# Optimization experiments

Hardware: AMD Instinct MI355X
Metric: run time of the kernel (lower is better)

Reference implementation:

```python
import jax, jax.numpy as jnp
import numpy as np

N_HEADS, D_MODEL, D_HEAD = 16, 1024, 64
INIT_STD = 0.02


def setup_inputs() -> dict:
    key = jax.random.key(0)
    ks = jax.random.split(key, 5)
    x = jax.random.normal(ks[0], (4, 2048, D_MODEL), dtype=jnp.float32)
    W_Q = jax.random.normal(ks[1], (N_HEADS, D_MODEL, D_HEAD), dtype=jnp.float32) * INIT_STD
    W_K = jax.random.normal(ks[2], (N_HEADS, D_MODEL, D_HEAD), dtype=jnp.float32) * INIT_STD
    W_V = jax.random.normal(ks[3], (N_HEADS, D_MODEL, D_HEAD), dtype=jnp.float32) * INIT_STD
    W_O = jax.random.normal(ks[4], (N_HEADS, D_HEAD, D_MODEL), dtype=jnp.float32) * INIT_STD
    b_Q = jnp.zeros((N_HEADS, D_HEAD), dtype=jnp.float32)
    b_K = jnp.zeros((N_HEADS, D_HEAD), dtype=jnp.float32)
    b_V = jnp.zeros((N_HEADS, D_HEAD), dtype=jnp.float32)
    b_O = jnp.zeros((D_MODEL,), dtype=jnp.float32)
    return {"normalized_resid_pre": x, "W_Q": W_Q, "W_K": W_K, "W_V": W_V,
            "W_O": W_O, "b_Q": b_Q, "b_K": b_K, "b_V": b_V, "b_O": b_O}


def reference(normalized_resid_pre, W_Q, W_K, W_V, W_O, b_Q, b_K, b_V, b_O):
    x = normalized_resid_pre  # [b, s, d_model]
    q = jnp.einsum('bsm,hmd->bshd', x, W_Q) + b_Q  # [b, s, h, d_head]
    k = jnp.einsum('bsm,hmd->bshd', x, W_K) + b_K
    v = jnp.einsum('bsm,hmd->bshd', x, W_V) + b_V
    scores = jnp.einsum('bqhd,bkhd->bhqk', q, k) / jnp.sqrt(jnp.float32(D_HEAD))
    S = x.shape[1]
    causal = jnp.tril(jnp.ones((S, S), dtype=bool))  # keep key_pos <= query_pos
    scores = jnp.where(causal, scores, jnp.finfo(scores.dtype).min)
    pattern = jax.nn.softmax(scores, axis=-1)  # [b, h, q, k]
    z = jnp.einsum('bhqk,bkhd->bqhd', pattern, v)
    attn_out = jnp.einsum('bqhd,hdm->bqm', z, W_O) + b_O
    return attn_out
```

## Files before the change

kernel.cpp:

```cpp
#include <hip/hip_runtime.h>
#include <hip/hip_bf16.h>
#include <math.h>

typedef __bf16 bf16_t;
typedef bf16_t bf16x8 __attribute__((ext_vector_type(8)));
typedef float f32x4 __attribute__((ext_vector_type(4)));

#define BB 4
#define SS 2048
#define HH 16
#define DMODEL 1024
#define DHEAD 64

__device__ inline unsigned short f2bf(float f) {
    union { __hip_bfloat16 h; unsigned short u; } cvt;
    cvt.h = __float2bfloat16(f);
    return cvt.u;
}

__device__ __forceinline__ void gll16(const unsigned short* g, unsigned short* l) {
    __builtin_amdgcn_global_load_lds(
        (const __attribute__((address_space(1))) unsigned int*)(g),
        (__attribute__((address_space(3))) unsigned int*)(l), 16, 0, 0);
}


__global__ void pack_x(const float* __restrict__ x, unsigned short* __restrict__ xb) {
    int i = blockIdx.x * 256 + threadIdx.x;
    const float4 v = ((const float4*)x)[i];
    unsigned short o[4] = { f2bf(v.x), f2bf(v.y), f2bf(v.z), f2bf(v.w) };
    *(uint2*)(xb + 4 * (size_t)i) = *(uint2*)o;
}

__global__ void pack_wqkv(const float* __restrict__ wq, const float* __restrict__ wk,
                          const float* __restrict__ wv, unsigned short* __restrict__ out) {
    int idx = blockIdx.x * 256 + threadIdx.x;
    int k  = idx & 1023;
    int n  = idx >> 10;
    int mat = n >> 10;
    int n1 = n & 1023;
    int h = n1 >> 6, d = n1 & 63;
    const float* w = (mat == 0) ? wq : (mat == 1) ? wk : wv;
    out[idx] = f2bf(w[(h << 16) + (k << 6) + d]);
}

__global__ void pack_wo(const float* __restrict__ wo, unsigned short* __restrict__ out) {
    int idx = blockIdx.x * 256 + threadIdx.x;
    int k = idx & 1023, n = idx >> 10;
    out[idx] = f2bf(wo[(k << 10) + n]);
}


__global__ __launch_bounds__(256) void gemm_qkv(
    const unsigned short* __restrict__ xb,
    const unsigned short* __restrict__ wT,
    const float* __restrict__ bq, const float* __restrict__ bk, const float* __restrict__ bv,
    unsigned short* __restrict__ qws, unsigned short* __restrict__ kws,
    unsigned short* __restrict__ vtw)
{
    __shared__ __align__(16) unsigned short lA[128 * 32];
    __shared__ __align__(16) unsigned short lB[128 * 32];
    const int t = threadIdx.x;
    const int lane = t & 63;
    const int w = t >> 6;
    const int quad = lane >> 4;
    const int l15 = lane & 15;
    const int n0 = blockIdx.x * 128;
    const int m0 = blockIdx.y * 128;
    const int wm = (w >> 1) * 64;
    const int wn = (w & 1) * 64;
    const int mat = n0 >> 10;

    f32x4 acc[4][4] = {};

    const int srow = w * 16 + (lane >> 2);
    const int scol = (lane & 3) * 8;
    const unsigned short* Ag0 = xb + (size_t)(m0 + srow) * 1024 + scol;
    const unsigned short* Ag1 = Ag0 + (size_t)64 * 1024;
    const unsigned short* Bg0 = wT + (size_t)(n0 + srow) * 1024 + scol;
    const unsigned short* Bg1 = Bg0 + (size_t)64 * 1024;
    unsigned short* lA0 = lA + (w * 16) * 32;
    unsigned short* lA1 = lA + (64 + w * 16) * 32;
    unsigned short* lB0 = lB + (w * 16) * 32;
    unsigned short* lB1 = lB + (64 + w * 16) * 32;

    if (mat != 2) {
        for (int kt = 0; kt < 1024; kt += 32) {
            __syncthreads();
            gll16(Ag0 + kt, lA0);
            gll16(Ag1 + kt, lA1);
            gll16(Bg0 + kt, lB0);
            gll16(Bg1 + kt, lB1);
            __syncthreads();
            bf16x8 af[4], bfr[4];
#pragma unroll
            for (int i = 0; i < 4; i++) {
                af[i]  = *(const bf16x8*)(lA + (wm + i * 16 + l15) * 32 + quad * 8);
                bfr[i] = *(const bf16x8*)(lB + (wn + i * 16 + l15) * 32 + quad * 8);
            }
#pragma unroll
            for (int i = 0; i < 4; i++)
#pragma unroll
                for (int j = 0; j < 4; j++)
                    acc[i][j] = __builtin_amdgcn_mfma_f32_16x16x32_bf16(bfr[j], af[i], acc[i][j], 0, 0, 0);
        }
        const int b = m0 >> 11;
        const float* bias_p = (mat == 0) ? bq : bk;
        unsigned short* dst = (mat == 0) ? qws : kws;
        const float qscale = (mat == 0) ? 0.125f : 1.0f;
#pragma unroll
        for (int j = 0; j < 4; j++) {
            const int noff = wn + j * 16 + quad * 4;
            const int h = noff >> 6;
            const int hglob = ((n0 & 1023) >> 6) + h;
            const int dbase = noff & 63;
            const float4 bv4 = *(const float4*)(bias_p + hglob * 64 + dbase);
            const float bias_r[4] = { bv4.x, bv4.y, bv4.z, bv4.w };
#pragma unroll
            for (int i = 0; i < 4; i++) {
                const int s = (m0 & 2047) + wm + i * 16 + l15;
                unsigned short pk[4];
#pragma unroll
                for (int r = 0; r < 4; r++) pk[r] = f2bf((acc[i][j][r] + bias_r[r]) * qscale);
                *(uint2*)(dst + (size_t)((b * 16 + hglob) * 2048 + s) * 64 + dbase) = *(uint2*)pk;
            }
        }
    } else {
        for (int kt = 0; kt < 1024; kt += 32) {
            __syncthreads();
            gll16(Ag0 + kt, lA0);
            gll16(Ag1 + kt, lA1);
            gll16(Bg0 + kt, lB0);
            gll16(Bg1 + kt, lB1);
            __syncthreads();
            bf16x8 af[4], bfr[4];
#pragma unroll
            for (int i = 0; i < 4; i++) {
                af[i]  = *(const bf16x8*)(lA + (wm + i * 16 + l15) * 32 + quad * 8);
                bfr[i] = *(const bf16x8*)(lB + (wn + i * 16 + l15) * 32 + quad * 8);
            }
#pragma unroll
            for (int i = 0; i < 4; i++)
#pragma unroll
                for (int j = 0; j < 4; j++)
                    acc[i][j] = __builtin_amdgcn_mfma_f32_16x16x32_bf16(af[i], bfr[j], acc[i][j], 0, 0, 0);
        }
        const int b = m0 >> 11;
#pragma unroll
        for (int j = 0; j < 4; j++) {
            const int n1 = (n0 & 1023) + wn + j * 16 + l15;
            const int h = n1 >> 6, d = n1 & 63;
            const float bias = bv[h * 64 + d];
#pragma unroll
            for (int i = 0; i < 4; i++) {
                const int s0 = (m0 & 2047) + wm + i * 16 + quad * 4;
                unsigned short pk[4];
#pragma unroll
                for (int r = 0; r < 4; r++) pk[r] = f2bf(acc[i][j][r] + bias);
                *(uint2*)(vtw + ((size_t)(b * 16 + h) * 64 + d) * 2048 + s0) = *(uint2*)pk;
            }
        }
    }
}


__global__ __launch_bounds__(256) void attn5(
    const unsigned short* __restrict__ qws,
    const unsigned short* __restrict__ kws,
    const unsigned short* __restrict__ vtw,
    unsigned short* __restrict__ zb)
{
    __shared__ __align__(16) unsigned short Ks[64 * 72];
    __shared__ __align__(16) unsigned short Vs[64 * 72];
    __shared__ __align__(16) unsigned short Ps[4 * 16 * 72];

    const int t = threadIdx.x;
    const int lane = t & 63;
    const int w = t >> 6;
    const int quad = lane >> 4;
    const int l15 = lane & 15;

    const int qt = 15 - (blockIdx.x >> 6);
    const int bh = blockIdx.x & 63;
    const int q0 = qt * 128;
    const int qbase = q0 + w * 32;
    const size_t base = (size_t)bh * SS * DHEAD;
    const unsigned short* Q = qws + base;
    const unsigned short* K = kws + base;
    const unsigned short* Vt = vtw + base;

    bf16x8 qf[2][2];
#pragma unroll
    for (int qt_ = 0; qt_ < 2; qt_++) {
        const unsigned short* qp = Q + (size_t)(qbase + qt_ * 16 + l15) * 64 + quad * 8;
        qf[qt_][0] = *(const bf16x8*)(qp);
        qf[qt_][1] = *(const bf16x8*)(qp + 32);
    }

    f32x4 o[2][4] = {};
    float lsum[2] = {0.f, 0.f};
    unsigned short* Pw = Ps + w * 16 * 72;

    const int sr = t >> 2;
    const int sc = (t & 3) * 8;
    const int nch = qt * 2 + 2;

    for (int c = 0; c < nch; c++) {
        const int kb = c * 64;
        __syncthreads();
        {
            const unsigned short* kp = K + (size_t)(kb + sr) * 64 + sc;
            *(uint4*)(Ks + sr * 72 + sc)      = *(const uint4*)(kp);
            *(uint4*)(Ks + sr * 72 + sc + 32) = *(const uint4*)(kp + 32);
            const unsigned short* vp = Vt + (size_t)sr * 2048 + kb + sc;
            *(uint4*)(Vs + sr * 72 + sc)      = *(const uint4*)(vp);
            *(uint4*)(Vs + sr * 72 + sc + 32) = *(const uint4*)(vp + 32);
        }
        __syncthreads();

        if (kb > qbase + 31) continue;

        f32x4 st[2][4];
#pragma unroll
        for (int sub = 0; sub < 4; sub++) {
            const bf16x8 kf0 = *(const bf16x8*)(Ks + (sub * 16 + l15) * 72 + quad * 8);
            const bf16x8 kf1 = *(const bf16x8*)(Ks + (sub * 16 + l15) * 72 + 32 + quad * 8);
#pragma unroll
            for (int qt_ = 0; qt_ < 2; qt_++) {
                f32x4 sv = {};
                sv = __builtin_amdgcn_mfma_f32_16x16x32_bf16(kf0, qf[qt_][0], sv, 0, 0, 0);
                sv = __builtin_amdgcn_mfma_f32_16x16x32_bf16(kf1, qf[qt_][1], sv, 0, 0, 0);
                st[qt_][sub] = sv;
            }
        }

        uint2 pd[2][4];
        const bool edge = (kb + 63 > qbase);
#pragma unroll
        for (int qt_ = 0; qt_ < 2; qt_++) {
            const int qg = qbase + qt_ * 16 + l15;
            float psum = 0.f;
#pragma unroll
            for (int sub = 0; sub < 4; sub++) {
                float p[4];
#pragma unroll
                for (int r = 0; r < 4; r++) {
                    const int key = kb + sub * 16 + quad * 4 + r;
                    float v = __expf(st[qt_][sub][r]);
                    p[r] = (edge && key > qg) ? 0.f : v;
                    psum += p[r];
                }
                pd[qt_][sub].x = (unsigned)f2bf(p[0]) | ((unsigned)f2bf(p[1]) << 16);
                pd[qt_][sub].y = (unsigned)f2bf(p[2]) | ((unsigned)f2bf(p[3]) << 16);
            }
            lsum[qt_] += psum;
        }

        bf16x8 vf[2][4];
#pragma unroll
        for (int c0 = 0; c0 < 2; c0++)
#pragma unroll
            for (int dt = 0; dt < 4; dt++)
                vf[c0][dt] = *(const bf16x8*)(Vs + (dt * 16 + l15) * 72 + c0 * 32 + quad * 8);

#pragma unroll
        for (int qt_ = 0; qt_ < 2; qt_++) {
#pragma unroll
            for (int sub = 0; sub < 4; sub++)
                *(uint2*)(Pw + l15 * 72 + sub * 16 + quad * 4) = pd[qt_][sub];
            asm volatile("s_waitcnt lgkmcnt(0)" ::: "memory");
#pragma unroll
            for (int c0 = 0; c0 < 2; c0++) {
                const bf16x8 pf = *(const bf16x8*)(Pw + l15 * 72 + c0 * 32 + quad * 8);
#pragma unroll
                for (int dt = 0; dt < 4; dt++)
                    o[qt_][dt] = __builtin_amdgcn_mfma_f32_16x16x32_bf16(vf[c0][dt], pf, o[qt_][dt], 0, 0, 0);
            }
            if (qt_ == 0) asm volatile("s_waitcnt lgkmcnt(0)" ::: "memory");
        }
    }

    const int b = bh >> 4, h = bh & 15;
#pragma unroll
    for (int qt_ = 0; qt_ < 2; qt_++) {
        float v = lsum[qt_];
        v += __shfl_xor(v, 16);
        v += __shfl_xor(v, 32);
        const float inv = 1.0f / v;
        const int q = qbase + qt_ * 16 + l15;
        unsigned short* zrow = zb + (size_t)(b * 2048 + q) * 1024 + h * 64 + quad * 4;
#pragma unroll
        for (int dt = 0; dt < 4; dt++) {
            unsigned short pk[4];
#pragma unroll
            for (int r = 0; r < 4; r++) pk[r] = f2bf(o[qt_][dt][r] * inv);
            *(uint2*)(zrow + dt * 16) = *(uint2*)pk;
        }
    }
}


__global__ __launch_bounds__(256) void gemm_out(
    const unsigned short* __restrict__ zb,
    const unsigned short* __restrict__ wT,
    const float* __restrict__ bo,
    float* __restrict__ out)
{
    __shared__ __align__(16) unsigned short lA[128 * 32];
    __shared__ __align__(16) unsigned short lB[128 * 32];
    const int t = threadIdx.x;
    const int lane = t & 63;
    const int w = t >> 6;
    const int quad = lane >> 4;
    const int l15 = lane & 15;
    const int n0 = blockIdx.x * 128;
    const int m0 = blockIdx.y * 128;
    const int wm = (w >> 1) * 64;
    const int wn = (w & 1) * 64;

    f32x4 acc[4][4] = {};

    const int srow = w * 16 + (lane >> 2);
    const int scol = (lane & 3) * 8;
    const unsigned short* Ag0 = zb + (size_t)(m0 + srow) * 1024 + scol;
    const unsigned short* Ag1 = Ag0 + (size_t)64 * 1024;
    const unsigned short* Bg0 = wT + (size_t)(n0 + srow) * 1024 + scol;
    const unsigned short* Bg1 = Bg0 + (size_t)64 * 1024;
    unsigned short* lA0 = lA + (w * 16) * 32;
    unsigned short* lA1 = lA + (64 + w * 16) * 32;
    unsigned short* lB0 = lB + (w * 16) * 32;
    unsigned short* lB1 = lB + (64 + w * 16) * 32;

    for (int kt = 0; kt < 1024; kt += 32) {
        __syncthreads();
        gll16(Ag0 + kt, lA0);
        gll16(Ag1 + kt, lA1);
        gll16(Bg0 + kt, lB0);
        gll16(Bg1 + kt, lB1);
        __syncthreads();
        bf16x8 af[4], bfr[4];
#pragma unroll
        for (int i = 0; i < 4; i++) {
            af[i]  = *(const bf16x8*)(lA + (wm + i * 16 + l15) * 32 + quad * 8);
            bfr[i] = *(const bf16x8*)(lB + (wn + i * 16 + l15) * 32 + quad * 8);
        }
#pragma unroll
        for (int i = 0; i < 4; i++)
#pragma unroll
            for (int j = 0; j < 4; j++)
                acc[i][j] = __builtin_amdgcn_mfma_f32_16x16x32_bf16(bfr[j], af[i], acc[i][j], 0, 0, 0);
    }

#pragma unroll
    for (int j = 0; j < 4; j++) {
        const int nbase = n0 + wn + j * 16 + quad * 4;
        const float4 bv4 = *(const float4*)(bo + nbase);
#pragma unroll
        for (int i = 0; i < 4; i++) {
            const int s = m0 + wm + i * 16 + l15;
            float4 v;
            v.x = acc[i][j][0] + bv4.x;
            v.y = acc[i][j][1] + bv4.y;
            v.z = acc[i][j][2] + bv4.z;
            v.w = acc[i][j][3] + bv4.w;
            *(float4*)(out + (size_t)s * 1024 + nbase) = v;
        }
    }
}


extern "C" void kernel_launch(void* const* d_in, const int* in_sizes, int n_in,
                              void* d_out, int out_size, void* d_ws, size_t ws_size,
                              hipStream_t stream) {
    const float* x  = (const float*)d_in[0];
    const float* WQ = (const float*)d_in[1];
    const float* WK = (const float*)d_in[2];
    const float* WV = (const float*)d_in[3];
    const float* WO = (const float*)d_in[4];
    const float* bQ = (const float*)d_in[5];
    const float* bK = (const float*)d_in[6];
    const float* bV = (const float*)d_in[7];
    const float* bO = (const float*)d_in[8];
    float* out = (float*)d_out;

    char* ws = (char*)d_ws;
    unsigned short* xb   = (unsigned short*)ws;
    unsigned short* wqkv = (unsigned short*)(ws + (16u << 20));
    unsigned short* woT  = (unsigned short*)(ws + (22u << 20));
    unsigned short* qws  = (unsigned short*)(ws + (24u << 20));
    unsigned short* kws  = (unsigned short*)(ws + (40u << 20));
    unsigned short* vtw  = (unsigned short*)(ws + (56u << 20));
    unsigned short* zbuf = xb;

    pack_x<<<8192, 256, 0, stream>>>(x, xb);
    pack_wqkv<<<(3072 * 1024) / 256, 256, 0, stream>>>(WQ, WK, WV, wqkv);
    pack_wo<<<(1024 * 1024) / 256, 256, 0, stream>>>(WO, woT);
    gemm_qkv<<<dim3(24, 64), 256, 0, stream>>>(xb, wqkv, bQ, bK, bV, qws, kws, vtw);
    attn5<<<1024, 256, 0, stream>>>(qws, kws, vtw, zbuf);
    gemm_out<<<dim3(8, 64), 256, 0, stream>>>(zbuf, woT, bO, out);
}
```

Baseline: 293.0 us.

## Split attention keys across waves, tile weight packing, swizzle GEMM block order

The attention kernel now uses 64-query blocks where each wave handles an interleaved subset of 32-key chunks. Each wave has its own LDS region and needs no block-wide barriers in the main loop, and partial outputs and row sums are reduced through shared memory at the end. Softmax switches to exp2 with the log2e factor folded into the Q scale, and probabilities are packed to bf16 with a byte-permute instead of rounding. Weight packing becomes one LDS-tiled transpose kernel with coalesced reads and writes in place of two strided kernels. Both GEMMs use a 1D grid with grouped block ordering for L2 reuse. In exchange, the change adds an LDS reduction epilogue and uses truncating bf16 conversion for the probabilities.

```diff
diff --git a/kernel.cpp b/kernel.cpp
--- a/kernel.cpp
+++ b/kernel.cpp
@@ -11,11 +11,18 @@
 #define HH 16
 #define DMODEL 1024
 #define DHEAD 64
+#define QSCALE 0.18033688011112042f
 
 __device__ inline unsigned short f2bf(float f) {
     union { __hip_bfloat16 h; unsigned short u; } cvt;
     cvt.h = __float2bfloat16(f);
     return cvt.u;
+}
+
+__device__ __forceinline__ unsigned pack_bf2(float lo, float hi) {
+    unsigned a = __builtin_bit_cast(unsigned, lo);
+    unsigned b = __builtin_bit_cast(unsigned, hi);
+    return __builtin_amdgcn_perm(b, a, 0x07060302);
 }
 
 __device__ __forceinline__ void gll16(const unsigned short* g, unsigned short* l) {
@@ -32,22 +39,56 @@
     *(uint2*)(xb + 4 * (size_t)i) = *(uint2*)o;
 }
 
-__global__ void pack_wqkv(const float* __restrict__ wq, const float* __restrict__ wk,
-                          const float* __restrict__ wv, unsigned short* __restrict__ out) {
-    int idx = blockIdx.x * 256 + threadIdx.x;
-    int k  = idx & 1023;
-    int n  = idx >> 10;
-    int mat = n >> 10;
-    int n1 = n & 1023;
-    int h = n1 >> 6, d = n1 & 63;
-    const float* w = (mat == 0) ? wq : (mat == 1) ? wk : wv;
-    out[idx] = f2bf(w[(h << 16) + (k << 6) + d]);
-}
-
-__global__ void pack_wo(const float* __restrict__ wo, unsigned short* __restrict__ out) {
-    int idx = blockIdx.x * 256 + threadIdx.x;
-    int k = idx & 1023, n = idx >> 10;
-    out[idx] = f2bf(wo[(k << 10) + n]);
+__global__ __launch_bounds__(256) void pack_w(
+    const float* __restrict__ wq, const float* __restrict__ wk, const float* __restrict__ wv,
+    const float* __restrict__ wo, unsigned short* __restrict__ qkvT, unsigned short* __restrict__ woT)
+{
+    __shared__ unsigned short tile[64 * 72];
+    const int t = threadIdx.x;
+    const int bid = blockIdx.x;
+    const int r = t >> 2;
+    const int c4 = (t & 3) * 16;
+    if (bid < 768) {
+        const int mat = bid >> 8;
+        const int rem = bid & 255;
+        const int h = rem >> 4;
+        const int m0 = (rem & 15) * 64;
+        const float* w = (mat == 0) ? wq : (mat == 1) ? wk : wv;
+        const float* src = w + ((size_t)h << 16) + (size_t)(m0 + r) * 64 + c4;
+#pragma unroll
+        for (int k2 = 0; k2 < 4; k2++) {
+            float4 v = *(const float4*)(src + k2 * 4);
+            tile[(c4 + k2 * 4 + 0) * 72 + r] = f2bf(v.x);
+            tile[(c4 + k2 * 4 + 1) * 72 + r] = f2bf(v.y);
+            tile[(c4 + k2 * 4 + 2) * 72 + r] = f2bf(v.z);
+            tile[(c4 + k2 * 4 + 3) * 72 + r] = f2bf(v.w);
+        }
+        __syncthreads();
+        const int d = t >> 2;
+        const int rq = (t & 3) * 16;
+        unsigned short* dst = qkvT + (size_t)(mat * 1024 + h * 64 + d) * 1024 + m0 + rq;
+        *(uint4*)(dst)     = *(const uint4*)(tile + d * 72 + rq);
+        *(uint4*)(dst + 8) = *(const uint4*)(tile + d * 72 + rq + 8);
+    } else {
+        const int bid2 = bid - 768;
+        const int h = bid2 >> 4;
+        const int m0 = (bid2 & 15) * 64;
+        const float* src = wo + ((size_t)h << 16) + (size_t)r * 1024 + m0 + c4;
+#pragma unroll
+        for (int k2 = 0; k2 < 4; k2++) {
+            float4 v = *(const float4*)(src + k2 * 4);
+            tile[(c4 + k2 * 4 + 0) * 72 + r] = f2bf(v.x);
+            tile[(c4 + k2 * 4 + 1) * 72 + r] = f2bf(v.y);
+            tile[(c4 + k2 * 4 + 2) * 72 + r] = f2bf(v.z);
+            tile[(c4 + k2 * 4 + 3) * 72 + r] = f2bf(v.w);
+        }
+        __syncthreads();
+        const int m = t >> 2;
+        const int dq = (t & 3) * 16;
+        unsigned short* dst = woT + (size_t)(m0 + m) * 1024 + h * 64 + dq;
+        *(uint4*)(dst)     = *(const uint4*)(tile + m * 72 + dq);
+        *(uint4*)(dst + 8) = *(const uint4*)(tile + m * 72 + dq + 8);
+    }
 }
 
 
@@ -65,8 +106,11 @@
     const int w = t >> 6;
     const int quad = lane >> 4;
     const int l15 = lane & 15;
-    const int n0 = blockIdx.x * 128;
-    const int m0 = blockIdx.y * 128;
+    const int bid = blockIdx.x;
+    const int mb = (bid & 7) + ((bid / 192) << 3);
+    const int nb = (bid >> 3) % 24;
+    const int n0 = nb * 128;
+    const int m0 = mb * 128;
     const int wm = (w >> 1) * 64;
     const int wn = (w & 1) * 64;
     const int mat = n0 >> 10;
@@ -107,12 +151,11 @@
         const int b = m0 >> 11;
         const float* bias_p = (mat == 0) ? bq : bk;
         unsigned short* dst = (mat == 0) ? qws : kws;
-        const float qscale = (mat == 0) ? 0.125f : 1.0f;
+        const float qscale = (mat == 0) ? QSCALE : 1.0f;
 #pragma unroll
         for (int j = 0; j < 4; j++) {
             const int noff = wn + j * 16 + quad * 4;
-            const int h = noff >> 6;
-            const int hglob = ((n0 & 1023) >> 6) + h;
+            const int hglob = ((n0 & 1023) >> 6) + (noff >> 6);
             const int dbase = noff & 63;
             const float4 bv4 = *(const float4*)(bias_p + hglob * 64 + dbase);
             const float bias_r[4] = { bv4.x, bv4.y, bv4.z, bv4.w };
@@ -164,137 +207,169 @@
 }
 
 
-__global__ __launch_bounds__(256) void attn5(
+#define AR_SZ 9984
+
+__global__ __launch_bounds__(256) void attn6(
     const unsigned short* __restrict__ qws,
     const unsigned short* __restrict__ kws,
     const unsigned short* __restrict__ vtw,
     unsigned short* __restrict__ zb)
 {
-    __shared__ __align__(16) unsigned short Ks[64 * 72];
-    __shared__ __align__(16) unsigned short Vs[64 * 72];
-    __shared__ __align__(16) unsigned short Ps[4 * 16 * 72];
-
+    __shared__ __align__(16) unsigned char smem[4 * AR_SZ];
     const int t = threadIdx.x;
     const int lane = t & 63;
     const int w = t >> 6;
     const int quad = lane >> 4;
     const int l15 = lane & 15;
 
-    const int qt = 15 - (blockIdx.x >> 6);
+    const int qt = 31 - (blockIdx.x >> 6);
     const int bh = blockIdx.x & 63;
-    const int q0 = qt * 128;
-    const int qbase = q0 + w * 32;
+    const int q0 = qt * 64;
     const size_t base = (size_t)bh * SS * DHEAD;
     const unsigned short* Q = qws + base;
     const unsigned short* K = kws + base;
     const unsigned short* Vt = vtw + base;
 
-    bf16x8 qf[2][2];
-#pragma unroll
-    for (int qt_ = 0; qt_ < 2; qt_++) {
-        const unsigned short* qp = Q + (size_t)(qbase + qt_ * 16 + l15) * 64 + quad * 8;
-        qf[qt_][0] = *(const bf16x8*)(qp);
-        qf[qt_][1] = *(const bf16x8*)(qp + 32);
-    }
-
-    f32x4 o[2][4] = {};
-    float lsum[2] = {0.f, 0.f};
-    unsigned short* Pw = Ps + w * 16 * 72;
-
-    const int sr = t >> 2;
-    const int sc = (t & 3) * 8;
-    const int nch = qt * 2 + 2;
-
-    for (int c = 0; c < nch; c++) {
-        const int kb = c * 64;
-        __syncthreads();
+    unsigned short* Ks = (unsigned short*)(smem + w * AR_SZ);
+    unsigned short* Vs = (unsigned short*)(smem + w * AR_SZ + 4608);
+    unsigned short* Pw = (unsigned short*)(smem + w * AR_SZ + 8704);
+
+    bf16x8 qf[4][2];
+#pragma unroll
+    for (int i = 0; i < 4; i++) {
+        const unsigned short* qp = Q + (size_t)(q0 + i * 16 + l15) * 64 + quad * 8;
+        qf[i][0] = *(const bf16x8*)qp;
+        qf[i][1] = *(const bf16x8*)(qp + 32);
+    }
+
+    f32x4 o[4][4] = {};
+    f32x4 lsum = {0.f, 0.f, 0.f, 0.f};
+
+    const int nch = 2 * qt + 2;
+    const int krow = lane >> 1;
+    const int kcol = (lane & 1) * 32;
+
+    for (int c = w; c < nch; c += 4) {
+        const int kb = c * 32;
+#pragma unroll
+        for (int g = 0; g < 4; g++)
+            gll16(Vt + (size_t)(g * 16 + (lane >> 2)) * 2048 + kb + (lane & 3) * 8, Vs + g * 512);
         {
-            const unsigned short* kp = K + (size_t)(kb + sr) * 64 + sc;
-            *(uint4*)(Ks + sr * 72 + sc)      = *(const uint4*)(kp);
-            *(uint4*)(Ks + sr * 72 + sc + 32) = *(const uint4*)(kp + 32);
-            const unsigned short* vp = Vt + (size_t)sr * 2048 + kb + sc;
-            *(uint4*)(Vs + sr * 72 + sc)      = *(const uint4*)(vp);
-            *(uint4*)(Vs + sr * 72 + sc + 32) = *(const uint4*)(vp + 32);
-        }
-        __syncthreads();
-
-        if (kb > qbase + 31) continue;
-
-        f32x4 st[2][4];
-#pragma unroll
-        for (int sub = 0; sub < 4; sub++) {
-            const bf16x8 kf0 = *(const bf16x8*)(Ks + (sub * 16 + l15) * 72 + quad * 8);
-            const bf16x8 kf1 = *(const bf16x8*)(Ks + (sub * 16 + l15) * 72 + 32 + quad * 8);
-#pragma unroll
-            for (int qt_ = 0; qt_ < 2; qt_++) {
-                f32x4 sv = {};
-                sv = __builtin_amdgcn_mfma_f32_16x16x32_bf16(kf0, qf[qt_][0], sv, 0, 0, 0);
-                sv = __builtin_amdgcn_mfma_f32_16x16x32_bf16(kf1, qf[qt_][1], sv, 0, 0, 0);
-                st[qt_][sub] = sv;
-            }
-        }
-
-        uint2 pd[2][4];
-        const bool edge = (kb + 63 > qbase);
-#pragma unroll
-        for (int qt_ = 0; qt_ < 2; qt_++) {
-            const int qg = qbase + qt_ * 16 + l15;
-            float psum = 0.f;
-#pragma unroll
-            for (int sub = 0; sub < 4; sub++) {
-                float p[4];
+            const unsigned short* kp = K + (size_t)(kb + krow) * 64 + kcol;
+            uint4 a0 = *(const uint4*)(kp);
+            uint4 a1 = *(const uint4*)(kp + 8);
+            uint4 a2 = *(const uint4*)(kp + 16);
+            uint4 a3 = *(const uint4*)(kp + 24);
+            unsigned short* kd = Ks + krow * 72 + kcol;
+            *(uint4*)(kd)      = a0;
+            *(uint4*)(kd + 8)  = a1;
+            *(uint4*)(kd + 16) = a2;
+            *(uint4*)(kd + 24) = a3;
+        }
+        asm volatile("s_waitcnt vmcnt(0) lgkmcnt(0)" ::: "memory");
+
+        bf16x8 kf[2][2];
+#pragma unroll
+        for (int ks = 0; ks < 2; ks++) {
+            kf[ks][0] = *(const bf16x8*)(Ks + (ks * 16 + l15) * 72 + quad * 8);
+            kf[ks][1] = *(const bf16x8*)(Ks + (ks * 16 + l15) * 72 + 32 + quad * 8);
+        }
+        bf16x8 vf[4];
+#pragma unroll
+        for (int dt = 0; dt < 4; dt++)
+            vf[dt] = *(const bf16x8*)(Vs + (dt * 16 + l15) * 32 + quad * 8);
+
+        const bool edge = (kb + 31 > q0);
+#pragma unroll
+        for (int qs = 0; qs < 4; qs++) {
+            if (edge && kb > q0 + qs * 16 + 15) continue;
+            f32x4 s0 = {}, s1 = {};
+            s0 = __builtin_amdgcn_mfma_f32_16x16x32_bf16(kf[0][0], qf[qs][0], s0, 0, 0, 0);
+            s0 = __builtin_amdgcn_mfma_f32_16x16x32_bf16(kf[0][1], qf[qs][1], s0, 0, 0, 0);
+            s1 = __builtin_amdgcn_mfma_f32_16x16x32_bf16(kf[1][0], qf[qs][0], s1, 0, 0, 0);
+            s1 = __builtin_amdgcn_mfma_f32_16x16x32_bf16(kf[1][1], qf[qs][1], s1, 0, 0, 0);
+            float p[8];
+            if (edge) {
+                const int qg = q0 + qs * 16 + l15;
 #pragma unroll
                 for (int r = 0; r < 4; r++) {
-                    const int key = kb + sub * 16 + quad * 4 + r;
-                    float v = __expf(st[qt_][sub][r]);
-                    p[r] = (edge && key > qg) ? 0.f : v;
-                    psum += p[r];
+                    p[r]     = (kb + quad * 4 + r      > qg) ? 0.f : exp2f(s0[r]);
+                    p[4 + r] = (kb + 16 + quad * 4 + r > qg) ? 0.f : exp2f(s1[r]);
                 }
-                pd[qt_][sub].x = (unsigned)f2bf(p[0]) | ((unsigned)f2bf(p[1]) << 16);
-                pd[qt_][sub].y = (unsigned)f2bf(p[2]) | ((unsigned)f2bf(p[3]) << 16);
-            }
-            lsum[qt_] += psum;
-        }
-
-        bf16x8 vf[2][4];
-#pragma unroll
-        for (int c0 = 0; c0 < 2; c0++)
+            } else {
+#pragma unroll
+                for (int r = 0; r < 4; r++) { p[r] = exp2f(s0[r]); p[4 + r] = exp2f(s1[r]); }
+            }
+            lsum[qs] += p[0] + p[1] + p[2] + p[3] + p[4] + p[5] + p[6] + p[7];
+            uint2 d0, d1;
+            d0.x = pack_bf2(p[0], p[1]); d0.y = pack_bf2(p[2], p[3]);
+            d1.x = pack_bf2(p[4], p[5]); d1.y = pack_bf2(p[6], p[7]);
+            *(uint2*)(Pw + l15 * 40 + quad * 4)      = d0;
+            *(uint2*)(Pw + l15 * 40 + 16 + quad * 4) = d1;
+            asm volatile("s_waitcnt lgkmcnt(0)" ::: "memory");
+            bf16x8 pf = *(const bf16x8*)(Pw + l15 * 40 + quad * 8);
 #pragma unroll
             for (int dt = 0; dt < 4; dt++)
-                vf[c0][dt] = *(const bf16x8*)(Vs + (dt * 16 + l15) * 72 + c0 * 32 + quad * 8);
-
-#pragma unroll
-        for (int qt_ = 0; qt_ < 2; qt_++) {
-#pragma unroll
-            for (int sub = 0; sub < 4; sub++)
-                *(uint2*)(Pw + l15 * 72 + sub * 16 + quad * 4) = pd[qt_][sub];
+                o[qs][dt] = __builtin_amdgcn_mfma_f32_16x16x32_bf16(vf[dt], pf, o[qs][dt], 0, 0, 0);
             asm volatile("s_waitcnt lgkmcnt(0)" ::: "memory");
-#pragma unroll
-            for (int c0 = 0; c0 < 2; c0++) {
-                const bf16x8 pf = *(const bf16x8*)(Pw + l15 * 72 + c0 * 32 + quad * 8);
-#pragma unroll
-                for (int dt = 0; dt < 4; dt++)
-                    o[qt_][dt] = __builtin_amdgcn_mfma_f32_16x16x32_bf16(vf[c0][dt], pf, o[qt_][dt], 0, 0, 0);
-            }
-            if (qt_ == 0) asm volatile("s_waitcnt lgkmcnt(0)" ::: "memory");
-        }
-    }
-
-    const int b = bh >> 4, h = bh & 15;
-#pragma unroll
-    for (int qt_ = 0; qt_ < 2; qt_++) {
-        float v = lsum[qt_];
-        v += __shfl_xor(v, 16);
-        v += __shfl_xor(v, 32);
-        const float inv = 1.0f / v;
-        const int q = qbase + qt_ * 16 + l15;
-        unsigned short* zrow = zb + (size_t)(b * 2048 + q) * 1024 + h * 64 + quad * 4;
-#pragma unroll
-        for (int dt = 0; dt < 4; dt++) {
-            unsigned short pk[4];
-#pragma unroll
-            for (int r = 0; r < 4; r++) pk[r] = f2bf(o[qt_][dt][r] * inv);
-            *(uint2*)(zrow + dt * 16) = *(uint2*)pk;
+        }
+    }
+
+    float* R0 = (float*)(smem);
+    float* R1 = (float*)(smem + 17408);
+    __syncthreads();
+    if (w & 1) {
+        float* R = (w == 1) ? R0 : R1;
+#pragma unroll
+        for (int i = 0; i < 4; i++)
+#pragma unroll
+            for (int j = 0; j < 4; j++)
+                *(f32x4*)(R + ((i * 4 + j) * 64 + lane) * 4) = o[i][j];
+        *(f32x4*)(R + 4096 + lane * 4) = lsum;
+    }
+    __syncthreads();
+    if (!(w & 1)) {
+        float* R = (w == 0) ? R0 : R1;
+#pragma unroll
+        for (int i = 0; i < 4; i++)
+#pragma unroll
+            for (int j = 0; j < 4; j++)
+                o[i][j] += *(const f32x4*)(R + ((i * 4 + j) * 64 + lane) * 4);
+        lsum += *(const f32x4*)(R + 4096 + lane * 4);
+    }
+    __syncthreads();
+    if (w == 2) {
+#pragma unroll
+        for (int i = 0; i < 4; i++)
+#pragma unroll
+            for (int j = 0; j < 4; j++)
+                *(f32x4*)(R0 + ((i * 4 + j) * 64 + lane) * 4) = o[i][j];
+        *(f32x4*)(R0 + 4096 + lane * 4) = lsum;
+    }
+    __syncthreads();
+    if (w == 0) {
+#pragma unroll
+        for (int i = 0; i < 4; i++)
+#pragma unroll
+            for (int j = 0; j < 4; j++)
+                o[i][j] += *(const f32x4*)(R0 + ((i * 4 + j) * 64 + lane) * 4);
+        lsum += *(const f32x4*)(R0 + 4096 + lane * 4);
+        const int b = bh >> 4, h = bh & 15;
+#pragma unroll
+        for (int i = 0; i < 4; i++) {
+            float v = lsum[i];
+            v += __shfl_xor(v, 16);
+            v += __shfl_xor(v, 32);
+            const float inv = 1.0f / v;
+            const int q = q0 + i * 16 + l15;
+            unsigned short* zr = zb + (size_t)(b * 2048 + q) * 1024 + h * 64 + quad * 4;
+#pragma unroll
+            for (int dt = 0; dt < 4; dt++) {
+                unsigned short pk[4];
+#pragma unroll
+                for (int r = 0; r < 4; r++) pk[r] = f2bf(o[i][dt][r] * inv);
+                *(uint2*)(zr + dt * 16) = *(uint2*)pk;
+            }
         }
     }
 }
@@ -313,8 +388,11 @@
     const int w = t >> 6;
     const int quad = lane >> 4;
     const int l15 = lane & 15;
-    const int n0 = blockIdx.x * 128;
-    const int m0 = blockIdx.y * 128;
+    const int bid = blockIdx.x;
+    const int mb = (bid & 7) + ((bid >> 6) << 3);
+    const int nb = (bid >> 3) & 7;
+    const int n0 = nb * 128;
+    const int m0 = mb * 128;
     const int wm = (w >> 1) * 64;
     const int wn = (w & 1) * 64;
 
@@ -393,9 +471,8 @@
     unsigned short* zbuf = xb;
 
     pack_x<<<8192, 256, 0, stream>>>(x, xb);
-    pack_wqkv<<<(3072 * 1024) / 256, 256, 0, stream>>>(WQ, WK, WV, wqkv);
-    pack_wo<<<(1024 * 1024) / 256, 256, 0, stream>>>(WO, woT);
-    gemm_qkv<<<dim3(24, 64), 256, 0, stream>>>(xb, wqkv, bQ, bK, bV, qws, kws, vtw);
-    attn5<<<1024, 256, 0, stream>>>(qws, kws, vtw, zbuf);
-    gemm_out<<<dim3(8, 64), 256, 0, stream>>>(zbuf, woT, bO, out);
-}
+    pack_w<<<1024, 256, 0, stream>>>(WQ, WK, WV, WO, wqkv, woT);
+    gemm_qkv<<<1536, 256, 0, stream>>>(xb, wqkv, bQ, bK, bV, qws, kws, vtw);
+    attn6<<<2048, 256, 0, stream>>>(qws, kws, vtw, zbuf);
+    gemm_out<<<512, 256, 0, stream>>>(zbuf, woT, bO, out);
+}
```

After: 293.5 us. No clear change (+0.2%).
